# Kernel tuning notes

Measured on AMD Instinct MI355X. Metric: run time of the kernel, lower is better.

The kernel has to match this reference:

```python
import jax, jax.numpy as jnp
import numpy as np

# ---- static config (matches init_kwargs) ----
L = 8          # multipath taps
DECAY = 4.0
N = 512        # batch
P = 1
M_SUB = 64     # opt.M
K_CP = 16      # opt.K
N_PILOT = 2
NS = 62
S = NS + N_PILOT            # 64  (OFDM, is_pb)
M = M_SUB + K_CP + N_PILOT  # 82
SMK = S * M                 # 5248
CARRIER = 3.6e9
SCS = 15e3
C_LIGHT = 3e8


def setup_inputs() -> dict:
    key = jax.random.key(0)
    k1, k2, k3, k4, k5 = jax.random.split(key, 5)
    eps = 1e-6
    return {
        "input_real": jax.random.normal(k1, (N, P, SMK), jnp.float32),
        "input_imag": jax.random.normal(k2, (N, P, SMK), jnp.float32),
        "ray_u": jax.random.uniform(k3, (N, P, L), jnp.float32, eps, 1.0 - eps),
        "angles_u": jax.random.uniform(k4, (L,), jnp.float32),
        "phase_u": jax.random.uniform(k5, (N, P, L, 1), jnp.float32),
        "velocity": 30,
        "Ns": NS,
    }


def _channel(input_real, input_imag, ray_u, angles_u, phase_u, velocity, Ns):
    S_ = Ns + N_PILOT  # == S
    two_pi = 2.0 * np.pi
    x = (input_real + 1j * input_imag).astype(jnp.complex64)

    # tap power profile and Rayleigh fading gains (rayleigh(u)=sqrt(-2 ln u))
    power = jnp.exp(-jnp.arange(L, dtype=jnp.float32) / DECAY)
    power = power / jnp.sum(power)
    cof = jnp.sqrt(power / 2.0) * jnp.sqrt(-2.0 * jnp.log(ray_u))  # (N,P,L)
    cof = -jnp.sort(-cof, axis=-1)  # descending sort

    # Doppler phase ramp: phases = (2*pi*cos(angle)*f_d + phi0) * t
    t = jnp.arange(S_, dtype=jnp.float32) / SCS  # (S,)
    fd = jnp.float32(velocity) / C_LIGHT * CARRIER
    doppler = two_pi * jnp.cos(angles_u * two_pi) * fd        # (L,)
    ph0 = doppler[None, None, :, None] + phase_u * two_pi      # (N,P,L,1)
    phases = ph0 * t[None, None, None, :]                      # (N,P,L,S)
    shift = jnp.exp(1j * phases).astype(jnp.complex64)
    cof_fin = cof[..., None].astype(jnp.complex64) * shift     # (N,P,L,S)

    # per-path time-varying gain applied to the OFDM grid
    xr = x.reshape(N, P, 1, S_, M)
    out = xr * cof_fin[..., None]                              # (N,P,L,S,M)

    # batch_conv1d with flipped eye / L == delay path l by l samples, scale 1/L
    T = S_ * M
    y = out.reshape(N, P, L, T)
    yp = jnp.pad(y, ((0, 0), (0, 0), (0, 0), (L - 1, 0)))      # (N,P,L,T+L-1)
    idx = (L - 1) - jnp.arange(L)[:, None] + jnp.arange(T)[None, :]  # (L,T)
    yd = jnp.take_along_axis(yp, idx[None, None], axis=-1) / L

    output = jnp.sum(yd, axis=2).reshape(N, P, SMK)            # complex64
    H_t = jnp.sum(cof_fin, axis=2).squeeze()                   # (N,S) complex64
    return output, H_t


def reference(input_real, input_imag, ray_u, angles_u, phase_u, velocity, Ns):
    return _channel(input_real, input_imag, ray_u, angles_u, phase_u, velocity, Ns)
```

## Files before the change

kernel.cpp:

```cpp
#include <hip/hip_runtime.h>
#include <hip/hip_bf16.h>


#define CH_L 8
#define CH_N 512
#define CH_S 64
#define CH_M 82
#define CH_T 5248
#define QSPLIT 4
#define GROUPS_PER_BLK 164
#define TILE_SLOTS 17

#define TWO_PI 6.283185307179586f

__device__ __forceinline__ unsigned pack_bf16x2(float lo, float hi) {
    __hip_bfloat16 hl = __float2bfloat16(lo);
    __hip_bfloat16 hh = __float2bfloat16(hi);
    unsigned short ul = *reinterpret_cast<unsigned short*>(&hl);
    unsigned short uh = *reinterpret_cast<unsigned short*>(&hh);
    return (unsigned)ul | ((unsigned)uh << 16);
}

__global__ __launch_bounds__(64) void prep_kernel(
    const float* __restrict__ ray_u,
    const float* __restrict__ angles_u,
    const float* __restrict__ phase_u,
    const void*  __restrict__ vel_raw,
    float2*      __restrict__ cf_ws,
    __hip_bfloat16* __restrict__ out)
{
    const int n   = blockIdx.x;
    const int tid = threadIdx.x;

    __shared__ float s_c[CH_L];
    __shared__ float s_ph0[CH_L];

    if (tid < CH_L) {
        float psum = 0.0f;
        #pragma unroll
        for (int l = 0; l < CH_L; ++l) psum += expf(-(float)l / 4.0f);
        float pw = expf(-(float)tid / 4.0f);
        float u  = ray_u[n * CH_L + tid];
        s_c[tid] = sqrtf(pw / (2.0f * psum)) * sqrtf(-2.0f * logf(u));
    }
    __syncthreads();
    if (tid == 0) {
        float c[CH_L];
        #pragma unroll
        for (int l = 0; l < CH_L; ++l) c[l] = s_c[l];
        for (int i = 1; i < CH_L; ++i) {
            float v = c[i];
            int j = i - 1;
            while (j >= 0 && c[j] < v) { c[j + 1] = c[j]; --j; }
            c[j + 1] = v;
        }
        #pragma unroll
        for (int l = 0; l < CH_L; ++l) s_c[l] = c[l];
    }
    __syncthreads();
    if (tid < CH_L) {
        const int   vi = *reinterpret_cast<const int*>(vel_raw);
        const float vf = *reinterpret_cast<const float*>(vel_raw);
        float vel;
        if (vi != 0 && vi > -1000000 && vi < 1000000) vel = (float)vi;
        else if (vf == vf && fabsf(vf) > 1e-3f && fabsf(vf) < 1e6f) vel = vf;
        else vel = 30.0f;
        const float fd = vel * (1.0f / 3.0e8f) * 3.6e9f;
        float ang = angles_u[tid] * TWO_PI;
        s_ph0[tid] = TWO_PI * cosf(ang) * fd + phase_u[n * CH_L + tid] * TWO_PI;
    }
    __syncthreads();

    const float ts = (float)tid * (1.0f / 15000.0f);
    float hr = 0.0f, hi = 0.0f;
    #pragma unroll
    for (int l = 0; l < CH_L; ++l) {
        float sn, cs;
        sincosf(s_ph0[l] * ts, &sn, &cs);
        float g = s_c[l];
        float2 v = make_float2(g * cs, g * sn);
        cf_ws[((size_t)n * CH_L + l) * CH_S + tid] = v;
        hr += v.x; hi += v.y;
    }
    size_t j = (size_t)CH_N * CH_T + (size_t)n * CH_S + tid;
    *reinterpret_cast<unsigned*>(&out[2 * j]) = pack_bf16x2(hi, hr);
}

__global__ __launch_bounds__(256) void conv_kernel(
    const float* __restrict__ xr,
    const float* __restrict__ xi,
    const float2* __restrict__ cf_ws,
    __hip_bfloat16* __restrict__ out)
{
    const int n   = blockIdx.x;
    const int q   = blockIdx.y;
    const int tid = threadIdx.x;

    __shared__ float2 tile[CH_L * TILE_SLOTS];

    if (tid < CH_L * TILE_SLOTS) {
        int l    = tid / TILE_SLOTS;
        int slot = tid - l * TILE_SLOTS;
        int s    = 16 * q - 1 + slot;
        float2 v = make_float2(0.0f, 0.0f);
        if (s >= 0) v = cf_ws[((size_t)n * CH_L + l) * CH_S + s];
        tile[tid] = v;
    }
    __syncthreads();

    if (tid >= GROUPS_PER_BLK) return;

    const float invL = 1.0f / (float)CH_L;
    const float* xrn = xr + (size_t)n * CH_T;
    const float* xin = xi + (size_t)n * CH_T;

    const int g  = q * GROUPS_PER_BLK + tid;
    const int t0 = g << 3;

    float wr[16], wi[16];
    if (t0 == 0) {
        #pragma unroll
        for (int k = 0; k < 8; ++k) { wr[k] = 0.0f; wi[k] = 0.0f; }
        float4 a = *reinterpret_cast<const float4*>(xrn);
        float4 b = *reinterpret_cast<const float4*>(xrn + 4);
        wr[8]=a.x; wr[9]=a.y; wr[10]=a.z; wr[11]=a.w;
        wr[12]=b.x; wr[13]=b.y; wr[14]=b.z; wr[15]=b.w;
        a = *reinterpret_cast<const float4*>(xin);
        b = *reinterpret_cast<const float4*>(xin + 4);
        wi[8]=a.x; wi[9]=a.y; wi[10]=a.z; wi[11]=a.w;
        wi[12]=b.x; wi[13]=b.y; wi[14]=b.z; wi[15]=b.w;
    } else {
        const float* pr = xrn + t0 - 8;
        float4 a = *reinterpret_cast<const float4*>(pr);
        float4 b = *reinterpret_cast<const float4*>(pr + 4);
        float4 c = *reinterpret_cast<const float4*>(pr + 8);
        float4 d = *reinterpret_cast<const float4*>(pr + 12);
        wr[0]=a.x; wr[1]=a.y; wr[2]=a.z; wr[3]=a.w;
        wr[4]=b.x; wr[5]=b.y; wr[6]=b.z; wr[7]=b.w;
        wr[8]=c.x; wr[9]=c.y; wr[10]=c.z; wr[11]=c.w;
        wr[12]=d.x; wr[13]=d.y; wr[14]=d.z; wr[15]=d.w;
        const float* pi = xin + t0 - 8;
        a = *reinterpret_cast<const float4*>(pi);
        b = *reinterpret_cast<const float4*>(pi + 4);
        c = *reinterpret_cast<const float4*>(pi + 8);
        d = *reinterpret_cast<const float4*>(pi + 12);
        wi[0]=a.x; wi[1]=a.y; wi[2]=a.z; wi[3]=a.w;
        wi[4]=b.x; wi[5]=b.y; wi[6]=b.z; wi[7]=b.w;
        wi[8]=c.x; wi[9]=c.y; wi[10]=c.z; wi[11]=c.w;
        wi[12]=d.x; wi[13]=d.y; wi[14]=d.z; wi[15]=d.w;
    }

    float rr[8], ii[8];
    #pragma unroll
    for (int k = 0; k < 8; ++k) {
        const int t     = t0 + k;
        const int s0    = t / CH_M;
        const int m0    = t - s0 * CH_M;
        const int slot0 = s0 - 16 * q + 1;
        float ar = 0.0f, ai = 0.0f;
        #pragma unroll
        for (int l = 0; l < CH_L; ++l) {
            int slot = (m0 >= l) ? slot0 : (slot0 - 1);
            float2 cf = tile[l * TILE_SLOTS + slot];
            float vr  = wr[8 + k - l];
            float vi2 = wi[8 + k - l];
            ar += vr * cf.x - vi2 * cf.y;
            ai += vr * cf.y + vi2 * cf.x;
        }
        rr[k] = ar * invL;
        ii[k] = ai * invL;
    }

    size_t base = 2 * ((size_t)n * CH_T + t0);
    uint4 v0, v1;
    v0.x = pack_bf16x2(ii[0], rr[0]); v0.y = pack_bf16x2(ii[1], rr[1]);
    v0.z = pack_bf16x2(ii[2], rr[2]); v0.w = pack_bf16x2(ii[3], rr[3]);
    v1.x = pack_bf16x2(ii[4], rr[4]); v1.y = pack_bf16x2(ii[5], rr[5]);
    v1.z = pack_bf16x2(ii[6], rr[6]); v1.w = pack_bf16x2(ii[7], rr[7]);
    *reinterpret_cast<uint4*>(&out[base])     = v0;
    *reinterpret_cast<uint4*>(&out[base + 8]) = v1;
}

extern "C" void kernel_launch(void* const* d_in, const int* in_sizes, int n_in,
                              void* d_out, int out_size, void* d_ws, size_t ws_size,
                              hipStream_t stream) {
    const float* xr       = (const float*)d_in[0];
    const float* xi       = (const float*)d_in[1];
    const float* ray_u    = (const float*)d_in[2];
    const float* angles_u = (const float*)d_in[3];
    const float* phase_u  = (const float*)d_in[4];
    const void*  velocity = d_in[5];

    __hip_bfloat16* out = (__hip_bfloat16*)d_out;
    float2* cf_ws = (float2*)d_ws;

    prep_kernel<<<CH_N, 64, 0, stream>>>(ray_u, angles_u, phase_u, velocity,
                                         cf_ws, out);
    dim3 grid(CH_N, QSPLIT);
    conv_kernel<<<grid, 256, 0, stream>>>(xr, xi, cf_ws, out);
}
```

Before: 19.85 us.

## Flatten conv grid to full 256-thread blocks and load coefficients into registers

The conv kernel now uses a flat 1D grid where every thread maps to one 8-sample group. Before, the grid was (batch, 4) with only 164 of 256 threads active per block, and each block staged coefficients through shared memory behind a barrier. Each thread now loads the two symbol rows of per-tap coefficients it needs straight from global memory into registers and picks between them per sample. The prep kernel also switches to fast intrinsic exp/log/cos/sincos, which trades some accuracy for cheaper math. Redundant global coefficient loads per thread replace the shared-memory reuse.

Result: faster. 19.32 us (-2.7%).

```diff
diff --git a/kernel.cpp b/kernel.cpp
--- a/kernel.cpp
+++ b/kernel.cpp
@@ -7,9 +7,8 @@
 #define CH_S 64
 #define CH_M 82
 #define CH_T 5248
-#define QSPLIT 4
-#define GROUPS_PER_BLK 164
-#define TILE_SLOTS 17
+#define GROUPS_N 656
+#define CONV_BLOCKS 1312
 
 #define TWO_PI 6.283185307179586f
 
@@ -38,10 +37,10 @@
     if (tid < CH_L) {
         float psum = 0.0f;
         #pragma unroll
-        for (int l = 0; l < CH_L; ++l) psum += expf(-(float)l / 4.0f);
-        float pw = expf(-(float)tid / 4.0f);
+        for (int l = 0; l < CH_L; ++l) psum += __expf(-(float)l / 4.0f);
+        float pw = __expf(-(float)tid / 4.0f);
         float u  = ray_u[n * CH_L + tid];
-        s_c[tid] = sqrtf(pw / (2.0f * psum)) * sqrtf(-2.0f * logf(u));
+        s_c[tid] = sqrtf(pw / (2.0f * psum)) * sqrtf(-2.0f * __logf(u));
     }
     __syncthreads();
     if (tid == 0) {
@@ -67,7 +66,7 @@
         else vel = 30.0f;
         const float fd = vel * (1.0f / 3.0e8f) * 3.6e9f;
         float ang = angles_u[tid] * TWO_PI;
-        s_ph0[tid] = TWO_PI * cosf(ang) * fd + phase_u[n * CH_L + tid] * TWO_PI;
+        s_ph0[tid] = TWO_PI * __cosf(ang) * fd + phase_u[n * CH_L + tid] * TWO_PI;
     }
     __syncthreads();
 
@@ -76,7 +75,7 @@
     #pragma unroll
     for (int l = 0; l < CH_L; ++l) {
         float sn, cs;
-        sincosf(s_ph0[l] * ts, &sn, &cs);
+        __sincosf(s_ph0[l] * ts, &sn, &cs);
         float g = s_c[l];
         float2 v = make_float2(g * cs, g * sn);
         cf_ws[((size_t)n * CH_L + l) * CH_S + tid] = v;
@@ -92,30 +91,27 @@
     const float2* __restrict__ cf_ws,
     __hip_bfloat16* __restrict__ out)
 {
-    const int n   = blockIdx.x;
-    const int q   = blockIdx.y;
-    const int tid = threadIdx.x;
+    const int g  = blockIdx.x * 256 + threadIdx.x;
+    const int n  = g / GROUPS_N;
+    const int gg = g - n * GROUPS_N;
+    const int t0 = gg << 3;
 
-    __shared__ float2 tile[CH_L * TILE_SLOTS];
+    const int s00 = t0 / CH_M;
+    const int m00 = t0 - s00 * CH_M;
+    const int sHi = s00 + ((m00 + 7) >= CH_M ? 1 : 0);
+    int sLo = s00 - (m00 < 7 ? 1 : 0);
+    if (sLo < 0) sLo = 0;
 
-    if (tid < CH_L * TILE_SLOTS) {
-        int l    = tid / TILE_SLOTS;
-        int slot = tid - l * TILE_SLOTS;
-        int s    = 16 * q - 1 + slot;
-        float2 v = make_float2(0.0f, 0.0f);
-        if (s >= 0) v = cf_ws[((size_t)n * CH_L + l) * CH_S + s];
-        tile[tid] = v;
+    const float2* cfn = cf_ws + (size_t)n * (CH_L * CH_S);
+    float2 flo[CH_L], fhi[CH_L];
+    #pragma unroll
+    for (int l = 0; l < CH_L; ++l) {
+        flo[l] = cfn[(l << 6) + sLo];
+        fhi[l] = cfn[(l << 6) + sHi];
     }
-    __syncthreads();
 
-    if (tid >= GROUPS_PER_BLK) return;
-
-    const float invL = 1.0f / (float)CH_L;
     const float* xrn = xr + (size_t)n * CH_T;
     const float* xin = xi + (size_t)n * CH_T;
-
-    const int g  = q * GROUPS_PER_BLK + tid;
-    const int t0 = g << 3;
 
     float wr[16], wi[16];
     if (t0 == 0) {
@@ -153,22 +149,22 @@
     float rr[8], ii[8];
     #pragma unroll
     for (int k = 0; k < 8; ++k) {
-        const int t     = t0 + k;
-        const int s0    = t / CH_M;
-        const int m0    = t - s0 * CH_M;
-        const int slot0 = s0 - 16 * q + 1;
+        int m = m00 + k;
+        int cross = (m >= CH_M) ? 1 : 0;
+        m -= cross * CH_M;
+        const int  s0   = s00 + cross;
+        const bool hi_t = (s0 == sHi);
         float ar = 0.0f, ai = 0.0f;
         #pragma unroll
         for (int l = 0; l < CH_L; ++l) {
-            int slot = (m0 >= l) ? slot0 : (slot0 - 1);
-            float2 cf = tile[l * TILE_SLOTS + slot];
+            float2 cf = (hi_t && (m >= l)) ? fhi[l] : flo[l];
             float vr  = wr[8 + k - l];
             float vi2 = wi[8 + k - l];
             ar += vr * cf.x - vi2 * cf.y;
             ai += vr * cf.y + vi2 * cf.x;
         }
-        rr[k] = ar * invL;
-        ii[k] = ai * invL;
+        rr[k] = ar * 0.125f;
+        ii[k] = ai * 0.125f;
     }
 
     size_t base = 2 * ((size_t)n * CH_T + t0);
@@ -196,6 +192,5 @@
 
     prep_kernel<<<CH_N, 64, 0, stream>>>(ray_u, angles_u, phase_u, velocity,
                                          cf_ws, out);
-    dim3 grid(CH_N, QSPLIT);
-    conv_kernel<<<grid, 256, 0, stream>>>(xr, xi, cf_ws, out);
+    conv_kernel<<<CONV_BLOCKS, 256, 0, stream>>>(xr, xi, cf_ws, out);
 }
```
